# Kernel optimization log

Measured on AMD Instinct MI355X. Metric: run time of the kernel, lower is better.

## Reference

```python
import jax, jax.numpy as jnp
import numpy as np

D_MODEL = 1024
N_HEADS = 16
WINDOW = 256
CAUSAL = True


def build_sliding_window_mask(T, window_size, causal=True):
    half = window_size // 2
    i = jnp.arange(T)[:, None]
    j = jnp.arange(T)[None, :]
    attend = jnp.abs(i - j) <= half
    if causal:
        attend = attend & (j <= i)
    return jnp.where(attend, 0.0, -jnp.inf).astype(jnp.float32)  # (T, T)


def setup_inputs() -> dict:
    key = jax.random.key(0)
    kx, kq, kk, kv, ko = jax.random.split(key, 5)
    B, T, D = 2, 2048, D_MODEL
    s = 1.0 / np.sqrt(D)
    return {
        "x": jax.random.normal(kx, (B, T, D), jnp.float32),
        "Wq": jax.random.normal(kq, (D, D), jnp.float32) * s,
        "Wk": jax.random.normal(kk, (D, D), jnp.float32) * s,
        "Wv": jax.random.normal(kv, (D, D), jnp.float32) * s,
        "Wo": jax.random.normal(ko, (D, D), jnp.float32) * s,
    }


def reference(x, Wq, Wk, Wv, Wo):
    B, T, D = x.shape
    H = N_HEADS
    dh = D // H
    # torch nn.Linear: y = x @ W.T
    def proj(W):
        return (x @ W.T).reshape(B, T, H, dh).transpose(0, 2, 1, 3)  # (B,H,T,dh)

    q, k, v = proj(Wq), proj(Wk), proj(Wv)
    scale = jnp.sqrt(jnp.asarray(dh, x.dtype))
    scores = jnp.einsum("bhtd,bhsd->bhts", q, k) / scale  # (B,H,T,T)
    mask = build_sliding_window_mask(T, WINDOW, CAUSAL)
    scores = scores + mask[None, None]
    attn = jax.nn.softmax(scores, axis=-1)
    attn = jnp.nan_to_num(attn, nan=0.0)
    out = jnp.einsum("bhts,bhsd->bhtd", attn, v)  # (B,H,T,dh)
    out = out.transpose(0, 2, 1, 3).reshape(B, T, D)
    return out @ Wo.T
```

## Files before the change

kernel.cpp:

```cpp
#include <hip/hip_runtime.h>
#include <hip/hip_bf16.h>

#define B_  2
#define T_  2048
#define D_  1024
#define H_  16
#define DH_ 64
#define M_  (B_ * T_)

typedef short s16x8 __attribute__((ext_vector_type(8)));
typedef float f32x4 __attribute__((ext_vector_type(4)));

__device__ inline float bfu(unsigned short u) {
    union { unsigned int i; float f; } c; c.i = ((unsigned int)u) << 16; return c.f;
}
__device__ inline unsigned short f2bf(float f) {
    union { float f; unsigned int i; } c; c.f = f;
    unsigned int r = c.i + 0x7fffu + ((c.i >> 16) & 1u);
    return (unsigned short)(r >> 16);
}
__device__ inline void stv(float* p, float v) { *p = v; }
__device__ inline void stv(unsigned short* p, float v) { *p = f2bf(v); }

__device__ inline void gload_lds16(const unsigned short* g, unsigned short* l) {
    __builtin_amdgcn_global_load_lds(
        (const __attribute__((address_space(1))) void*)g,
        (__attribute__((address_space(3))) void*)l, 16, 0, 0);
}

__global__ __launch_bounds__(256) void conv_bf16(const float* __restrict__ x,
                                                 const float* __restrict__ Wq,
                                                 const float* __restrict__ Wk,
                                                 const float* __restrict__ Wv,
                                                 const float* __restrict__ Wo,
                                                 unsigned short* __restrict__ dst) {
    const int g = blockIdx.x * 256 + threadIdx.x;
    const float* s; size_t o;
    if (g < (1 << 20)) { s = x; o = (size_t)g; }
    else {
        int gg = g - (1 << 20);
        int w = gg >> 18;
        o = (size_t)(gg & ((1 << 18) - 1));
        s = (w == 0) ? Wq : (w == 1) ? Wk : (w == 2) ? Wv : Wo;
    }
    float4 v = ((const float4*)s)[o];
    ushort4 u;
    u.x = f2bf(v.x); u.y = f2bf(v.y); u.z = f2bf(v.z); u.w = f2bf(v.w);
    ((ushort4*)dst)[g] = u;
}

template <typename Tout>
__global__ __launch_bounds__(256) void gemm_m97(const unsigned short* __restrict__ A,
                                                const unsigned short* __restrict__ Bw,
                                                Tout* __restrict__ C0,
                                                Tout* __restrict__ C1,
                                                Tout* __restrict__ C2,
                                                int K) {
    __shared__ unsigned short As[128 * 32];
    __shared__ unsigned short Bs[128 * 32];
    const int tid  = threadIdx.x;
    const int lane = tid & 63;
    const int wave = tid >> 6;
    const int wr = wave >> 1, wc = wave & 1;
    const int bm = blockIdx.y * 128, bn = blockIdx.x * 128;
    const int fr = lane & 15, kg = lane >> 4;
    const int lrow = lane >> 2;
    const int lcol = (lane & 3) * 8;

    f32x4 acc[4][4];
    #pragma unroll
    for (int mi = 0; mi < 4; ++mi)
        #pragma unroll
        for (int ni = 0; ni < 4; ++ni)
            #pragma unroll
            for (int r = 0; r < 4; ++r) acc[mi][ni][r] = 0.f;

    const unsigned short* ga = A  + (size_t)(bm + wave * 16 + lrow) * K + lcol;
    const unsigned short* gb = Bw + (size_t)(bn + wave * 16 + lrow) * K + lcol;
    unsigned short* la = &As[(wave * 16) * 32];
    unsigned short* lb = &Bs[(wave * 16) * 32];

    for (int k0 = 0; k0 < K; k0 += 32) {
        __syncthreads();
        gload_lds16(ga + k0,                 la);
        gload_lds16(ga + k0 + (size_t)64 * K, la + 64 * 32);
        gload_lds16(gb + k0,                 lb);
        gload_lds16(gb + k0 + (size_t)64 * K, lb + 64 * 32);
        __syncthreads();
        s16x8 af[4], bfv[4];
        #pragma unroll
        for (int mi = 0; mi < 4; ++mi)
            af[mi] = *(const s16x8*)&As[(wr * 64 + mi * 16 + fr) * 32 + kg * 8];
        #pragma unroll
        for (int ni = 0; ni < 4; ++ni)
            bfv[ni] = *(const s16x8*)&Bs[(wc * 64 + ni * 16 + fr) * 32 + kg * 8];
        #pragma unroll
        for (int mi = 0; mi < 4; ++mi)
            #pragma unroll
            for (int ni = 0; ni < 4; ++ni)
                acc[mi][ni] = __builtin_amdgcn_mfma_f32_16x16x32_bf16(af[mi], bfv[ni], acc[mi][ni], 0, 0, 0);
    }

    Tout* C = (bn < 1024) ? C0 : (bn < 2048) ? C1 : C2;
    const int nb = bn & 1023;
    #pragma unroll
    for (int mi = 0; mi < 4; ++mi)
        #pragma unroll
        for (int ni = 0; ni < 4; ++ni)
            #pragma unroll
            for (int r = 0; r < 4; ++r) {
                int m = bm + wr * 64 + mi * 16 + kg * 4 + r;
                int n = nb + wc * 64 + ni * 16 + fr;
                stv(&C[(size_t)m * 1024 + n], acc[mi][ni][r]);
            }
}

__global__ __launch_bounds__(256) void transpose_bh(const unsigned short* __restrict__ src0,
                                                    unsigned short* __restrict__ dst) {
    __shared__ unsigned short sm[64][66];
    const int tid = threadIdx.x;
    const int t0 = blockIdx.x * 64;
    const int bh = blockIdx.y;
    const int b = bh >> 4, h = bh & 15;
    const unsigned short* src = src0 + ((size_t)(b * T_ + t0)) * D_ + h * 64;
    #pragma unroll
    for (int kc = 0; kc < 16; ++kc) {
        int idx = kc * 256 + tid;
        int r = idx >> 6, c = idx & 63;
        sm[r][c] = src[(size_t)r * D_ + c];
    }
    __syncthreads();
    unsigned short* d2 = dst + (size_t)bh * 64 * T_ + t0;
    #pragma unroll
    for (int kc = 0; kc < 16; ++kc) {
        int idx = kc * 256 + tid;
        int d = idx >> 6, tt = idx & 63;
        d2[(size_t)d * T_ + tt] = sm[tt][d];
    }
}

__global__ __launch_bounds__(256) void swa_mfma(const unsigned short* qb,
                                                const unsigned short* __restrict__ kb,
                                                const unsigned short* __restrict__ vt,
                                                unsigned short* ob) {
    __shared__ unsigned short Pl[4][16 * 168];
    const int wave = threadIdx.x >> 6;
    const int lane = threadIdx.x & 63;
    const int qt = blockIdx.x * 4 + wave;
    const int i0 = (qt & (T_ / 16 - 1)) * 16;
    const int bh = qt >> 7;
    const int h = bh & (H_ - 1), b = bh >> 4;
    const int g = lane >> 4, l15 = lane & 15;

    const size_t rowbase = (size_t)b * T_ * D_ + (size_t)h * DH_;
    const int klo = (i0 > 128) ? (i0 - 128) : 0;

    unsigned short* Pw = Pl[wave];
    {
        int row = lane >> 2, col = 144 + (lane & 3) * 4;
        *(uint2*)&Pw[row * 168 + col] = make_uint2(0u, 0u);
    }

    const unsigned short* qrow = qb + rowbase + (size_t)(i0 + l15) * D_ + g * 8;
    const s16x8 aq0 = *(const s16x8*)(qrow);
    const s16x8 aq1 = *(const s16x8*)(qrow + 32);

    f32x4 sacc[9];
    #pragma unroll
    for (int t = 0; t < 9; ++t)
        #pragma unroll
        for (int r = 0; r < 4; ++r) sacc[t][r] = 0.f;

    const unsigned short* kbase = kb + rowbase;
    #pragma unroll
    for (int t = 0; t < 9; ++t) {
        const unsigned short* krow = kbase + (size_t)(klo + t * 16 + l15) * D_ + g * 8;
        s16x8 b0 = *(const s16x8*)(krow);
        s16x8 b1 = *(const s16x8*)(krow + 32);
        sacc[t] = __builtin_amdgcn_mfma_f32_16x16x32_bf16(aq0, b0, sacc[t], 0, 0, 0);
        sacc[t] = __builtin_amdgcn_mfma_f32_16x16x32_bf16(aq1, b1, sacc[t], 0, 0, 0);
    }

    float mrow[4] = {-1e30f, -1e30f, -1e30f, -1e30f};
    #pragma unroll
    for (int t = 0; t < 9; ++t)
        #pragma unroll
        for (int r = 0; r < 4; ++r) {
            const int j  = klo + t * 16 + l15;
            const int iq = i0 + g * 4 + r;
            const bool valid = (j <= iq) && (j + 128 >= iq);
            const float s = valid ? sacc[t][r] * 0.125f : -1e30f;
            sacc[t][r] = s;
            mrow[r] = fmaxf(mrow[r], s);
        }
    #pragma unroll
    for (int r = 0; r < 4; ++r)
        #pragma unroll
        for (int off = 1; off < 16; off <<= 1)
            mrow[r] = fmaxf(mrow[r], __shfl_xor(mrow[r], off));

    float lrow[4] = {0.f, 0.f, 0.f, 0.f};
    #pragma unroll
    for (int t = 0; t < 9; ++t)
        #pragma unroll
        for (int r = 0; r < 4; ++r) {
            const float p = __expf(sacc[t][r] - mrow[r]);
            sacc[t][r] = p;
            lrow[r] += p;
        }
    #pragma unroll
    for (int r = 0; r < 4; ++r) {
        #pragma unroll
        for (int off = 1; off < 16; off <<= 1)
            lrow[r] += __shfl_xor(lrow[r], off);
    }
    float invl[4];
    #pragma unroll
    for (int r = 0; r < 4; ++r) invl[r] = 1.f / lrow[r];

    #pragma unroll
    for (int t = 0; t < 9; ++t)
        #pragma unroll
        for (int r = 0; r < 4; ++r)
            Pw[(g * 4 + r) * 168 + t * 16 + l15] = f2bf(sacc[t][r]);

    f32x4 oacc[4];
    #pragma unroll
    for (int nt = 0; nt < 4; ++nt)
        #pragma unroll
        for (int r = 0; r < 4; ++r) oacc[nt][r] = 0.f;

    const unsigned short* vtb = vt + (size_t)bh * 64 * T_;
    #pragma unroll
    for (int kt = 0; kt < 5; ++kt) {
        const s16x8 ap = *(const s16x8*)&Pw[l15 * 168 + kt * 32 + g * 8];
        #pragma unroll
        for (int nt = 0; nt < 4; ++nt) {
            const unsigned short* vrow = vtb + (size_t)(nt * 16 + l15) * T_ + klo + kt * 32 + g * 8;
            s16x8 bv = *(const s16x8*)vrow;
            oacc[nt] = __builtin_amdgcn_mfma_f32_16x16x32_bf16(ap, bv, oacc[nt], 0, 0, 0);
        }
    }

    #pragma unroll
    for (int nt = 0; nt < 4; ++nt)
        #pragma unroll
        for (int r = 0; r < 4; ++r) {
            const float val = oacc[nt][r] * invl[r];
            ob[rowbase + (size_t)(i0 + g * 4 + r) * D_ + nt * 16 + l15] = f2bf(val);
        }
}

extern "C" void kernel_launch(void* const* d_in, const int* in_sizes, int n_in,
                              void* d_out, int out_size, void* d_ws, size_t ws_size,
                              hipStream_t stream) {
    const float* x  = (const float*)d_in[0];
    const float* Wq = (const float*)d_in[1];
    const float* Wk = (const float*)d_in[2];
    const float* Wv = (const float*)d_in[3];
    const float* Wo = (const float*)d_in[4];

    const size_t MD = (size_t)M_ * D_;
    const size_t WN = (size_t)D_ * D_;

    unsigned short* wsb = (unsigned short*)d_ws;
    unsigned short* xb  = wsb;
    unsigned short* Wqb = xb + MD;
    unsigned short* Wob = Wqb + 3 * WN;
    unsigned short* qb  = Wob + WN;
    unsigned short* vb  = qb + MD;
    unsigned short* vt = (unsigned short*)d_out;
    unsigned short* kb = vt + MD;

    conv_bf16<<<8192, 256, 0, stream>>>(x, Wq, Wk, Wv, Wo, wsb);

    gemm_m97<unsigned short><<<dim3(24, M_ / 128), 256, 0, stream>>>(
        xb, Wqb, qb, kb, vb, D_);
    transpose_bh<<<dim3(T_ / 64, B_ * H_), 256, 0, stream>>>(vb, vt);

    swa_mfma<<<(B_ * H_ * T_ / 16) / 4, 256, 0, stream>>>(qb, kb, vt, qb);

    gemm_m97<float><<<dim3(8, M_ / 128), 256, 0, stream>>>(
        qb, Wob, (float*)d_out, (float*)d_out, (float*)d_out, D_);
}
```

Before: 174.1 us.

## Share K tile in LDS across attention waves; shrink output GEMM M-tile

The sliding-window attention kernel now has each block handle 64 consecutive query rows of one head. The block loads the 192-row K window into shared memory once and all four waves read from it, instead of each wave fetching overlapping K rows from global memory. The GEMM kernel is templated on the M tile size, and the output projection uses BM=64, doubling its block count to improve occupancy and CU fill. The cost is an extra block-wide sync and larger LDS use in attention, plus lower per-block reuse in the output GEMM.

Result: faster. 164.2 us (-5.7%).

```diff
diff --git a/kernel.cpp b/kernel.cpp
--- a/kernel.cpp
+++ b/kernel.cpp
@@ -49,27 +49,28 @@
     ((ushort4*)dst)[g] = u;
 }
 
-template <typename Tout>
+template <int BM, typename Tout>
 __global__ __launch_bounds__(256) void gemm_m97(const unsigned short* __restrict__ A,
                                                 const unsigned short* __restrict__ Bw,
                                                 Tout* __restrict__ C0,
                                                 Tout* __restrict__ C1,
                                                 Tout* __restrict__ C2,
                                                 int K) {
-    __shared__ unsigned short As[128 * 32];
+    constexpr int MI = BM / 32;
+    __shared__ unsigned short As[BM * 32];
     __shared__ unsigned short Bs[128 * 32];
     const int tid  = threadIdx.x;
     const int lane = tid & 63;
     const int wave = tid >> 6;
     const int wr = wave >> 1, wc = wave & 1;
-    const int bm = blockIdx.y * 128, bn = blockIdx.x * 128;
+    const int bm = blockIdx.y * BM, bn = blockIdx.x * 128;
     const int fr = lane & 15, kg = lane >> 4;
     const int lrow = lane >> 2;
     const int lcol = (lane & 3) * 8;
 
-    f32x4 acc[4][4];
-    #pragma unroll
-    for (int mi = 0; mi < 4; ++mi)
+    f32x4 acc[MI][4];
+    #pragma unroll
+    for (int mi = 0; mi < MI; ++mi)
         #pragma unroll
         for (int ni = 0; ni < 4; ++ni)
             #pragma unroll
@@ -82,20 +83,21 @@
 
     for (int k0 = 0; k0 < K; k0 += 32) {
         __syncthreads();
-        gload_lds16(ga + k0,                 la);
-        gload_lds16(ga + k0 + (size_t)64 * K, la + 64 * 32);
-        gload_lds16(gb + k0,                 lb);
+        #pragma unroll
+        for (int s = 0; s < BM / 64; ++s)
+            gload_lds16(ga + k0 + (size_t)(s * 64) * K, la + s * 64 * 32);
+        gload_lds16(gb + k0,                  lb);
         gload_lds16(gb + k0 + (size_t)64 * K, lb + 64 * 32);
         __syncthreads();
-        s16x8 af[4], bfv[4];
-        #pragma unroll
-        for (int mi = 0; mi < 4; ++mi)
-            af[mi] = *(const s16x8*)&As[(wr * 64 + mi * 16 + fr) * 32 + kg * 8];
+        s16x8 af[MI], bfv[4];
+        #pragma unroll
+        for (int mi = 0; mi < MI; ++mi)
+            af[mi] = *(const s16x8*)&As[(wr * (BM / 2) + mi * 16 + fr) * 32 + kg * 8];
         #pragma unroll
         for (int ni = 0; ni < 4; ++ni)
             bfv[ni] = *(const s16x8*)&Bs[(wc * 64 + ni * 16 + fr) * 32 + kg * 8];
         #pragma unroll
-        for (int mi = 0; mi < 4; ++mi)
+        for (int mi = 0; mi < MI; ++mi)
             #pragma unroll
             for (int ni = 0; ni < 4; ++ni)
                 acc[mi][ni] = __builtin_amdgcn_mfma_f32_16x16x32_bf16(af[mi], bfv[ni], acc[mi][ni], 0, 0, 0);
@@ -104,12 +106,12 @@
     Tout* C = (bn < 1024) ? C0 : (bn < 2048) ? C1 : C2;
     const int nb = bn & 1023;
     #pragma unroll
-    for (int mi = 0; mi < 4; ++mi)
+    for (int mi = 0; mi < MI; ++mi)
         #pragma unroll
         for (int ni = 0; ni < 4; ++ni)
             #pragma unroll
             for (int r = 0; r < 4; ++r) {
-                int m = bm + wr * 64 + mi * 16 + kg * 4 + r;
+                int m = bm + wr * (BM / 2) + mi * 16 + kg * 4 + r;
                 int n = nb + wc * 64 + ni * 16 + fr;
                 stv(&C[(size_t)m * 1024 + n], acc[mi][ni][r]);
             }
@@ -139,21 +141,36 @@
     }
 }
 
-__global__ __launch_bounds__(256) void swa_mfma(const unsigned short* qb,
-                                                const unsigned short* __restrict__ kb,
-                                                const unsigned short* __restrict__ vt,
-                                                unsigned short* ob) {
+__global__ __launch_bounds__(256) void swa_mfma2(const unsigned short* qb,
+                                                 const unsigned short* __restrict__ kb,
+                                                 const unsigned short* __restrict__ vt,
+                                                 unsigned short* ob) {
+    __shared__ unsigned short Ks[192 * 64];
     __shared__ unsigned short Pl[4][16 * 168];
     const int wave = threadIdx.x >> 6;
     const int lane = threadIdx.x & 63;
-    const int qt = blockIdx.x * 4 + wave;
-    const int i0 = (qt & (T_ / 16 - 1)) * 16;
-    const int bh = qt >> 7;
+    const int blk = blockIdx.x;
+    const int i0b = (blk & 31) * 64;
+    const int bh  = blk >> 5;
     const int h = bh & (H_ - 1), b = bh >> 4;
     const int g = lane >> 4, l15 = lane & 15;
 
     const size_t rowbase = (size_t)b * T_ * D_ + (size_t)h * DH_;
+    const int klo2 = (i0b > 128) ? (i0b - 128) : 0;
+
+    {
+        const unsigned short* kg0 = kb + rowbase
+            + (size_t)(klo2 + (lane >> 3)) * D_ + (lane & 7) * 8;
+        #pragma unroll
+        for (int s = 0; s < 6; ++s) {
+            const int i = wave * 6 + s;
+            gload_lds16(kg0 + (size_t)(i * 8) * D_, &Ks[i * 8 * 64]);
+        }
+    }
+
+    const int i0  = i0b + wave * 16;
     const int klo = (i0 > 128) ? (i0 - 128) : 0;
+    const int koff = klo - klo2;
 
     unsigned short* Pw = Pl[wave];
     {
@@ -165,18 +182,19 @@
     const s16x8 aq0 = *(const s16x8*)(qrow);
     const s16x8 aq1 = *(const s16x8*)(qrow + 32);
 
+    __syncthreads();
+
     f32x4 sacc[9];
     #pragma unroll
     for (int t = 0; t < 9; ++t)
         #pragma unroll
         for (int r = 0; r < 4; ++r) sacc[t][r] = 0.f;
 
-    const unsigned short* kbase = kb + rowbase;
     #pragma unroll
     for (int t = 0; t < 9; ++t) {
-        const unsigned short* krow = kbase + (size_t)(klo + t * 16 + l15) * D_ + g * 8;
-        s16x8 b0 = *(const s16x8*)(krow);
-        s16x8 b1 = *(const s16x8*)(krow + 32);
+        const unsigned short* kr = &Ks[(koff + t * 16 + l15) * 64 + g * 8];
+        s16x8 b0 = *(const s16x8*)kr;
+        s16x8 b1 = *(const s16x8*)(kr + 32);
         sacc[t] = __builtin_amdgcn_mfma_f32_16x16x32_bf16(aq0, b0, sacc[t], 0, 0, 0);
         sacc[t] = __builtin_amdgcn_mfma_f32_16x16x32_bf16(aq1, b1, sacc[t], 0, 0, 0);
     }
@@ -274,12 +292,12 @@
 
     conv_bf16<<<8192, 256, 0, stream>>>(x, Wq, Wk, Wv, Wo, wsb);
 
-    gemm_m97<unsigned short><<<dim3(24, M_ / 128), 256, 0, stream>>>(
+    gemm_m97<128, unsigned short><<<dim3(24, M_ / 128), 256, 0, stream>>>(
         xb, Wqb, qb, kb, vb, D_);
     transpose_bh<<<dim3(T_ / 64, B_ * H_), 256, 0, stream>>>(vb, vt);
 
-    swa_mfma<<<(B_ * H_ * T_ / 16) / 4, 256, 0, stream>>>(qb, kb, vt, qb);
-
-    gemm_m97<float><<<dim3(8, M_ / 128), 256, 0, stream>>>(
+    swa_mfma2<<<(B_ * H_ * T_) / 64, 256, 0, stream>>>(qb, kb, vt, qb);
+
+    gemm_m97<64, float><<<dim3(8, M_ / 64), 256, 0, stream>>>(
         qb, Wob, (float*)d_out, (float*)d_out, (float*)d_out, D_);
 }
```
